# Kernel tuning notes

Hardware: AMD Instinct MI355X
Metric: run time of the kernel (lower is better)

The kernel has to match this reference:

```python
import jax, jax.numpy as jnp
import numpy as np

N = 8192      # number of graph nodes
C = 256       # feature_size
D = C // 2    # projection dim


def setup_inputs() -> dict:
    key = jax.random.key(0)
    ks = jax.random.split(key, 10)
    s_in = 1.0 / np.sqrt(C + 3)   # torch Linear default init scale (uniform bound)
    s_r = 1.0 / np.sqrt(D)
    return {
        "landmarks": jax.random.normal(ks[0], (1, N, 3), dtype=jnp.float32),
        "features": jax.random.normal(ks[1], (1, N, C), dtype=jnp.float32),
        # weights stored [in, out]
        "Wi": jax.random.uniform(ks[2], (C + 3, D), jnp.float32, -s_in, s_in),
        "bi": jax.random.uniform(ks[3], (D,), jnp.float32, -s_in, s_in),
        "Wj": jax.random.uniform(ks[4], (C + 3, D), jnp.float32, -s_in, s_in),
        "bj": jax.random.uniform(ks[5], (D,), jnp.float32, -s_in, s_in),
        "Wk": jax.random.uniform(ks[6], (C + 3, D), jnp.float32, -s_in, s_in),
        "bk": jax.random.uniform(ks[7], (D,), jnp.float32, -s_in, s_in),
        "Wr": jax.random.uniform(ks[8], (D, C), jnp.float32, -s_r, s_r),
        "br": jax.random.uniform(ks[9], (C,), jnp.float32, -s_r, s_r),
    }


def reference(landmarks, features, Wi, bi, Wj, bj, Wk, bk, Wr, br):
    # concat coords + features, drop the singleton batch dim: [N, C+3]
    x = jnp.concatenate([landmarks, features], axis=2)[0]
    fi = x @ Wi + bi                       # [N, D]
    fj = x @ Wj + bj                       # [N, D]
    fk = x @ Wk + bk                       # [N, D]
    att = jax.nn.sigmoid(fi @ fj.T)        # [N, N] sigmoid scores (non-softmax)
    att = att / jnp.sum(att, axis=1, keepdims=True)  # row-sum normalize
    out = (att @ fk) @ Wr + br             # [N, C] restored
    return features + out[None]            # residual, back to [1, N, C]
```

## Files before the change

kernel.cpp:

```cpp
#include <hip/hip_runtime.h>
#include <stdint.h>

#define N_NODES 8192
#define KPAD 272
#define OUTC 384

typedef __attribute__((ext_vector_type(8))) short bhalf8;
typedef __attribute__((ext_vector_type(16))) float f32x16;
typedef __attribute__((ext_vector_type(4))) float f32x4;

__device__ inline unsigned short f2bf_rne(float f) {
    unsigned u = __builtin_bit_cast(unsigned, f);
    u += 0x7FFFu + ((u >> 16) & 1u);
    return (unsigned short)(u >> 16);
}

__device__ inline bhalf8 mk8(unsigned a, unsigned b, unsigned c, unsigned d) {
    union { unsigned u[4]; bhalf8 v; } U;
    U.u[0] = a; U.u[1] = b; U.u[2] = c; U.u[3] = d;
    return U.v;
}

#define GLD_TO_LDS(gptr, lptr)                                                              \
    __builtin_amdgcn_global_load_lds((const __attribute__((address_space(1))) void*)(gptr), \
                                     (__attribute__((address_space(3))) void*)(lptr), 16, 0, 0)

__global__ void k_prep(const float* __restrict__ landmarks, const float* __restrict__ features,
                       const float* __restrict__ Wi, const float* __restrict__ bi,
                       const float* __restrict__ Wj, const float* __restrict__ bj,
                       const float* __restrict__ Wk, const float* __restrict__ bk,
                       const float* __restrict__ Wr,
                       unsigned short* __restrict__ xb, unsigned short* __restrict__ WcatT,
                       unsigned short* __restrict__ WrT, float* __restrict__ bcat) {
    int idx = blockIdx.x * 256 + threadIdx.x;
    const int XB_N = N_NODES * KPAD;
    const int WC_N = OUTC * KPAD;
    const int WR_N = 256 * 128;
    if (idx < XB_N) {
        int i = idx / KPAD, kk = idx - i * KPAD;
        float v = 0.f;
        if (kk < 256) v = features[i * 256 + kk];
        else if (kk < 259) v = landmarks[i * 3 + (kk - 256)];
        xb[idx] = f2bf_rne(v);
        return;
    }
    idx -= XB_N;
    if (idx < WC_N) {
        int n = idx / KPAD, kk = idx - n * KPAD;
        int sel = n >> 7, d = n & 127;
        const float* W = (sel == 0) ? Wi : ((sel == 1) ? Wj : Wk);
        float v = 0.f;
        if (kk < 256) v = W[(kk + 3) * 128 + d];
        else if (kk < 259) v = W[(kk - 256) * 128 + d];
        WcatT[idx] = f2bf_rne(v);
        return;
    }
    idx -= WC_N;
    if (idx < WR_N) {
        int c = idx >> 7, d = idx & 127;
        WrT[idx] = f2bf_rne(Wr[d * 256 + c]);
        return;
    }
    idx -= WR_N;
    if (idx < OUTC) {
        float v = (idx < 128) ? bi[idx] : ((idx < 256) ? bj[idx - 128] : bk[idx - 256]);
        bcat[idx] = v;
    }
}

__global__ __launch_bounds__(256) void k_proj(const unsigned short* __restrict__ xb,
                                              const unsigned short* __restrict__ WcatT,
                                              const float* __restrict__ bcat,
                                              unsigned short* __restrict__ fi,
                                              unsigned short* __restrict__ fj,
                                              unsigned short* __restrict__ fkT) {
    const int tid = threadIdx.x;
    const int w = tid >> 6, l = tid & 63, h = l >> 5, ln = l & 31;
    const int i0 = blockIdx.x * 32;
    f32x16 acc[3] = {};
#pragma unroll
    for (int s = 0; s < 17; ++s) {
        bhalf8 a = *(const bhalf8*)(xb + (size_t)(i0 + ln) * KPAD + s * 16 + h * 8);
#pragma unroll
        for (int t = 0; t < 3; ++t) {
            int n = 96 * w + 32 * t + ln;
            bhalf8 b = *(const bhalf8*)(WcatT + (size_t)n * KPAD + s * 16 + h * 8);
            acc[t] = __builtin_amdgcn_mfma_f32_32x32x16_bf16(a, b, acc[t], 0, 0, 0);
        }
    }
#pragma unroll
    for (int t = 0; t < 3; ++t) {
        int n = 96 * w + 32 * t + ln;
        int sel = n >> 7, d = n & 127;
        float bias = bcat[n];
#pragma unroll
        for (int q = 0; q < 4; ++q) {
            int ib = i0 + 8 * q + 4 * h;
            if (sel < 2) {
                unsigned short* dst = sel ? fj : fi;
#pragma unroll
                for (int r = 0; r < 4; ++r)
                    dst[(size_t)(ib + r) * 128 + d] = f2bf_rne(acc[t][4 * q + r] + bias);
            } else {
                ushort4 pk;
                pk.x = f2bf_rne(acc[t][4 * q + 0] + bias);
                pk.y = f2bf_rne(acc[t][4 * q + 1] + bias);
                pk.z = f2bf_rne(acc[t][4 * q + 2] + bias);
                pk.w = f2bf_rne(acc[t][4 * q + 3] + bias);
                *(ushort4*)(fkT + (size_t)d * N_NODES + ib) = pk;
            }
        }
    }
}

__global__ __launch_bounds__(256, 2) void k_attn(const unsigned short* __restrict__ fi,
                                                 const unsigned short* __restrict__ fj,
                                                 const unsigned short* __restrict__ fkT,
                                                 float* __restrict__ num_part,
                                                 float* __restrict__ den_part) {
    __shared__ __align__(16) char smem[65536];
    unsigned short* fj_s = (unsigned short*)smem;
    unsigned short* fk_s = (unsigned short*)(smem + 32768);
    float* bufA = (float*)smem;
    float* bufB = (float*)(smem + 17408);
    float* denb = (float*)(smem + 34816);

    const int tid = threadIdx.x;
    const int w = tid >> 6, l = tid & 63, h = l >> 5, ln = l & 31;
    const int rt = blockIdx.x & 127, jq = blockIdx.x >> 7;
    const int i0 = rt * 64;
    const int jbase = jq * 2048;

    bhalf8 bfi[2][8];
#pragma unroll
    for (int nt = 0; nt < 2; ++nt)
#pragma unroll
        for (int s = 0; s < 8; ++s)
            bfi[nt][s] = *(const bhalf8*)(fi + (size_t)(i0 + nt * 32 + ln) * 128 + s * 16 + h * 8);

    f32x16 acc[8] = {};
    float dacc0 = 0.f, dacc1 = 0.f;

    const int rsub = l >> 4;
    const int cph = l & 15;

    for (int mt = 0; mt < 16; ++mt) {
        const int j0 = jbase + mt * 128;
#pragma unroll
        for (int q = 0; q < 8; ++q) {
            int r = w * 32 + q * 4 + rsub;
            int c = cph ^ (r & 15);
            GLD_TO_LDS(fj + (size_t)(j0 + r) * 128 + c * 8, (char*)fj_s + (w * 32 + q * 4) * 256);
            GLD_TO_LDS(fkT + (size_t)r * N_NODES + j0 + c * 8, (char*)fk_s + (w * 32 + q * 4) * 256);
        }
        __syncthreads();

        f32x16 st0 = {}, st1 = {};
        const int jrow = w * 32 + ln;
#pragma unroll
        for (int s = 0; s < 8; ++s) {
            int c = (s * 2 + h) ^ (jrow & 15);
            bhalf8 af = *(const bhalf8*)((char*)fj_s + jrow * 256 + c * 16);
            st0 = __builtin_amdgcn_mfma_f32_32x32x16_bf16(af, bfi[0][s], st0, 0, 0, 0);
            st1 = __builtin_amdgcn_mfma_f32_32x32x16_bf16(af, bfi[1][s], st1, 0, 0, 0);
        }

        float sv0[16], sv1[16];
#pragma unroll
        for (int r = 0; r < 16; ++r) {
            float x0 = __builtin_amdgcn_rcpf(1.f + __builtin_amdgcn_exp2f(st0[r] * -1.44269504f));
            float x1 = __builtin_amdgcn_rcpf(1.f + __builtin_amdgcn_exp2f(st1[r] * -1.44269504f));
            dacc0 += x0; dacc1 += x1;
            sv0[r] = x0; sv1[r] = x1;
        }
        unsigned p0[8], p1[8], x0v[8], x1v[8];
#pragma unroll
        for (int q = 0; q < 8; ++q) {
            p0[q] = __builtin_amdgcn_perm(__builtin_bit_cast(unsigned, sv0[2 * q + 1]),
                                          __builtin_bit_cast(unsigned, sv0[2 * q]), 0x07060302u);
            p1[q] = __builtin_amdgcn_perm(__builtin_bit_cast(unsigned, sv1[2 * q + 1]),
                                          __builtin_bit_cast(unsigned, sv1[2 * q]), 0x07060302u);
        }
#pragma unroll
        for (int q = 0; q < 8; ++q) {
            x0v[q] = (unsigned)__shfl_xor((int)p0[q], 32, 64);
            x1v[q] = (unsigned)__shfl_xor((int)p1[q], 32, 64);
        }
        bhalf8 fb[2][2];
        if (h == 0) {
            fb[0][0] = mk8(p0[0], p0[1], x0v[0], x0v[1]);
            fb[0][1] = mk8(p0[4], p0[5], x0v[4], x0v[5]);
            fb[1][0] = mk8(p1[0], p1[1], x1v[0], x1v[1]);
            fb[1][1] = mk8(p1[4], p1[5], x1v[4], x1v[5]);
        } else {
            fb[0][0] = mk8(x0v[2], x0v[3], p0[2], p0[3]);
            fb[0][1] = mk8(x0v[6], x0v[7], p0[6], p0[7]);
            fb[1][0] = mk8(x1v[2], x1v[3], p1[2], p1[3]);
            fb[1][1] = mk8(x1v[6], x1v[7], p1[6], p1[7]);
        }
#pragma unroll
        for (int m4 = 0; m4 < 4; ++m4) {
#pragma unroll
            for (int s2 = 0; s2 < 2; ++s2) {
                int row = m4 * 32 + ln;
                int c = (w * 4 + s2 * 2 + h) ^ (row & 15);
                bhalf8 af = *(const bhalf8*)((char*)fk_s + row * 256 + c * 16);
                acc[m4 * 2 + 0] = __builtin_amdgcn_mfma_f32_32x32x16_bf16(af, fb[0][s2], acc[m4 * 2 + 0], 0, 0, 0);
                acc[m4 * 2 + 1] = __builtin_amdgcn_mfma_f32_32x32x16_bf16(af, fb[1][s2], acc[m4 * 2 + 1], 0, 0, 0);
            }
        }
        __syncthreads();
    }

    {
        float o0 = __shfl_xor(dacc0, 32, 64);
        float o1 = __shfl_xor(dacc1, 32, 64);
        dacc0 += o0; dacc1 += o1;
    }
    if (h == 0) {
        denb[w * 64 + ln] = dacc0;
        denb[w * 64 + 32 + ln] = dacc1;
    }

#pragma unroll
    for (int half = 0; half < 2; ++half) {
        __syncthreads();
        if (w < 2) {
            float* buf = w ? bufB : bufA;
#pragma unroll
            for (int m2 = 0; m2 < 2; ++m2) {
                int m4 = half * 2 + m2;
#pragma unroll
                for (int nt = 0; nt < 2; ++nt) {
                    int iloc = nt * 32 + ln;
#pragma unroll
                    for (int q = 0; q < 4; ++q) {
                        int d = m2 * 32 + 8 * q + 4 * h;
                        f32x4 v = {acc[m4 * 2 + nt][4 * q + 0], acc[m4 * 2 + nt][4 * q + 1],
                                   acc[m4 * 2 + nt][4 * q + 2], acc[m4 * 2 + nt][4 * q + 3]};
                        *(f32x4*)(buf + iloc * 68 + d) = v;
                    }
                }
            }
        }
        __syncthreads();
        if (w >= 2) {
            float* buf = (w == 3) ? bufB : bufA;
#pragma unroll
            for (int m2 = 0; m2 < 2; ++m2) {
                int m4 = half * 2 + m2;
#pragma unroll
                for (int nt = 0; nt < 2; ++nt) {
                    int iloc = nt * 32 + ln;
#pragma unroll
                    for (int q = 0; q < 4; ++q) {
                        int d = m2 * 32 + 8 * q + 4 * h;
                        f32x4 old = *(f32x4*)(buf + iloc * 68 + d);
                        f32x4 v = {acc[m4 * 2 + nt][4 * q + 0], acc[m4 * 2 + nt][4 * q + 1],
                                   acc[m4 * 2 + nt][4 * q + 2], acc[m4 * 2 + nt][4 * q + 3]};
                        *(f32x4*)(buf + iloc * 68 + d) = old + v;
                    }
                }
            }
        }
        __syncthreads();
#pragma unroll
        for (int e = 0; e < 4; ++e) {
            int v = e * 256 + tid;
            int iloc = v >> 4;
            int d4 = (v & 15) * 4;
            f32x4 s = *(f32x4*)(bufA + iloc * 68 + d4) + *(f32x4*)(bufB + iloc * 68 + d4);
            *(f32x4*)(num_part + (size_t)(jq * N_NODES + i0 + iloc) * 128 + half * 64 + d4) = s;
        }
    }
    __syncthreads();
    if (tid < 64) {
        den_part[(size_t)jq * N_NODES + i0 + tid] =
            denb[tid] + denb[64 + tid] + denb[128 + tid] + denb[192 + tid];
    }
}

__global__ void k_comb(const float* __restrict__ num_part, const float* __restrict__ den_part,
                       unsigned short* __restrict__ t) {
    int f = blockIdx.x * 256 + threadIdx.x;
    int i = f >> 5, d4 = (f & 31) * 4;
    f32x4 s = {};
    float ds = 0.f;
#pragma unroll
    for (int q = 0; q < 4; ++q) {
        s += *(const f32x4*)(num_part + (size_t)(q * N_NODES + i) * 128 + d4);
        ds += den_part[(size_t)q * N_NODES + i];
    }
    float inv = 1.0f / ds;
    ushort4 pk;
    pk.x = f2bf_rne(s.x * inv);
    pk.y = f2bf_rne(s.y * inv);
    pk.z = f2bf_rne(s.z * inv);
    pk.w = f2bf_rne(s.w * inv);
    *(ushort4*)(t + (size_t)i * 128 + d4) = pk;
}

__global__ __launch_bounds__(256) void k_out(const unsigned short* __restrict__ t,
                                             const unsigned short* __restrict__ WrT,
                                             const float* __restrict__ br,
                                             const float* __restrict__ features,
                                             float* __restrict__ out) {
    __shared__ __align__(16) char smem[65536];
    const int tid = threadIdx.x, w = tid >> 6, l = tid & 63, h = l >> 5, ln = l & 31;
    const int i0 = blockIdx.x * 32;
    {
        int rsub = l >> 4, cph = l & 15;
#pragma unroll
        for (int q = 0; q < 16; ++q) {
            int r = w * 64 + q * 4 + rsub;
            int c = cph ^ (r & 15);
            GLD_TO_LDS(WrT + (size_t)r * 128 + c * 8, (char*)smem + (w * 64 + q * 4) * 256);
        }
    }
    __syncthreads();
    f32x16 acc[2] = {};
#pragma unroll
    for (int s = 0; s < 8; ++s) {
        bhalf8 af = *(const bhalf8*)(t + (size_t)(i0 + ln) * 128 + s * 16 + h * 8);
#pragma unroll
        for (int nt = 0; nt < 2; ++nt) {
            int row = w * 64 + nt * 32 + ln;
            int c = (s * 2 + h) ^ (row & 15);
            bhalf8 bf = *(const bhalf8*)((char*)smem + row * 256 + c * 16);
            acc[nt] = __builtin_amdgcn_mfma_f32_32x32x16_bf16(af, bf, acc[nt], 0, 0, 0);
        }
    }
#pragma unroll
    for (int nt = 0; nt < 2; ++nt) {
        int cc = w * 64 + nt * 32 + ln;
        float bias = br[cc];
#pragma unroll
        for (int q = 0; q < 4; ++q) {
#pragma unroll
            for (int r = 0; r < 4; ++r) {
                int i = i0 + 8 * q + 4 * h + r;
                out[(size_t)i * 256 + cc] = acc[nt][4 * q + r] + bias + features[(size_t)i * 256 + cc];
            }
        }
    }
}

extern "C" void kernel_launch(void* const* d_in, const int* in_sizes, int n_in,
                              void* d_out, int out_size, void* d_ws, size_t ws_size,
                              hipStream_t stream) {
    const float* landmarks = (const float*)d_in[0];
    const float* features  = (const float*)d_in[1];
    const float* Wi = (const float*)d_in[2];
    const float* bi = (const float*)d_in[3];
    const float* Wj = (const float*)d_in[4];
    const float* bj = (const float*)d_in[5];
    const float* Wk = (const float*)d_in[6];
    const float* bk = (const float*)d_in[7];
    const float* Wr = (const float*)d_in[8];
    const float* br = (const float*)d_in[9];

    char* ws = (char*)d_ws;
    unsigned short* xb      = (unsigned short*)(ws + 0);
    unsigned short* WcatT   = (unsigned short*)(ws + 4456448);
    unsigned short* WrT     = (unsigned short*)(ws + 4665344);
    float*          bcat    = (float*)(ws + 4730880);
    unsigned short* fi      = (unsigned short*)(ws + 4732416);
    unsigned short* fjp     = (unsigned short*)(ws + 6829568);
    unsigned short* fkT     = (unsigned short*)(ws + 8926720);
    float*          num_part= (float*)(ws + 11023872);
    float*          den_part= (float*)(ws + 27801088);
    unsigned short* t       = (unsigned short*)(ws + 27932160);

    float* out = (float*)d_out;

    hipLaunchKernelGGL(k_prep, dim3(9242), dim3(256), 0, stream,
                       landmarks, features, Wi, bi, Wj, bj, Wk, bk, Wr, xb, WcatT, WrT, bcat);
    hipLaunchKernelGGL(k_proj, dim3(256), dim3(256), 0, stream, xb, WcatT, bcat, fi, fjp, fkT);
    hipLaunchKernelGGL(k_attn, dim3(512), dim3(256), 0, stream, fi, fjp, fkT, num_part, den_part);
    hipLaunchKernelGGL(k_comb, dim3(1024), dim3(256), 0, stream, num_part, den_part, t);
    hipLaunchKernelGGL(k_out, dim3(256), dim3(256), 0, stream, t, WrT, br, features, out);
}
```

Measured before the change: 183.5 us.

## Fuse input cast into projection, double-buffer attention, fold combine into output GEMM

```diff
diff --git a/kernel.cpp b/kernel.cpp
--- a/kernel.cpp
+++ b/kernel.cpp
@@ -25,26 +25,15 @@
     __builtin_amdgcn_global_load_lds((const __attribute__((address_space(1))) void*)(gptr), \
                                      (__attribute__((address_space(3))) void*)(lptr), 16, 0, 0)
 
-__global__ void k_prep(const float* __restrict__ landmarks, const float* __restrict__ features,
-                       const float* __restrict__ Wi, const float* __restrict__ bi,
+__global__ void k_prep(const float* __restrict__ Wi, const float* __restrict__ bi,
                        const float* __restrict__ Wj, const float* __restrict__ bj,
                        const float* __restrict__ Wk, const float* __restrict__ bk,
                        const float* __restrict__ Wr,
-                       unsigned short* __restrict__ xb, unsigned short* __restrict__ WcatT,
-                       unsigned short* __restrict__ WrT, float* __restrict__ bcat) {
+                       unsigned short* __restrict__ WcatT, unsigned short* __restrict__ WrT,
+                       float* __restrict__ bcat) {
     int idx = blockIdx.x * 256 + threadIdx.x;
-    const int XB_N = N_NODES * KPAD;
     const int WC_N = OUTC * KPAD;
     const int WR_N = 256 * 128;
-    if (idx < XB_N) {
-        int i = idx / KPAD, kk = idx - i * KPAD;
-        float v = 0.f;
-        if (kk < 256) v = features[i * 256 + kk];
-        else if (kk < 259) v = landmarks[i * 3 + (kk - 256)];
-        xb[idx] = f2bf_rne(v);
-        return;
-    }
-    idx -= XB_N;
     if (idx < WC_N) {
         int n = idx / KPAD, kk = idx - n * KPAD;
         int sel = n >> 7, d = n & 127;
@@ -68,47 +57,62 @@
     }
 }
 
-__global__ __launch_bounds__(256) void k_proj(const unsigned short* __restrict__ xb,
+__global__ __launch_bounds__(256) void k_proj(const float* __restrict__ landmarks,
+                                              const float* __restrict__ features,
                                               const unsigned short* __restrict__ WcatT,
                                               const float* __restrict__ bcat,
                                               unsigned short* __restrict__ fi,
                                               unsigned short* __restrict__ fj,
                                               unsigned short* __restrict__ fkT) {
-    const int tid = threadIdx.x;
-    const int w = tid >> 6, l = tid & 63, h = l >> 5, ln = l & 31;
-    const int i0 = blockIdx.x * 32;
-    f32x16 acc[3] = {};
+    const int tid = threadIdx.x, w = tid >> 6, l = tid & 63, h = l >> 5, ln = l & 31;
+    const unsigned bid = blockIdx.x;
+    const int it = bid / 3, ng = bid - it * 3;
+    const int i0 = it * 32;
+    const int n = ng * 128 + w * 32 + ln;
+    const int row = i0 + ln;
+    f32x16 acc = {};
 #pragma unroll
     for (int s = 0; s < 17; ++s) {
-        bhalf8 a = *(const bhalf8*)(xb + (size_t)(i0 + ln) * KPAD + s * 16 + h * 8);
-#pragma unroll
-        for (int t = 0; t < 3; ++t) {
-            int n = 96 * w + 32 * t + ln;
-            bhalf8 b = *(const bhalf8*)(WcatT + (size_t)n * KPAD + s * 16 + h * 8);
-            acc[t] = __builtin_amdgcn_mfma_f32_32x32x16_bf16(a, b, acc[t], 0, 0, 0);
-        }
-    }
-#pragma unroll
-    for (int t = 0; t < 3; ++t) {
-        int n = 96 * w + 32 * t + ln;
-        int sel = n >> 7, d = n & 127;
-        float bias = bcat[n];
+        union { unsigned short us[8]; bhalf8 v; } A;
+        if (s < 16) {
+            const float* fp = features + (size_t)row * 256 + s * 16 + h * 8;
+            f32x4 v0 = *(const f32x4*)(fp);
+            f32x4 v1 = *(const f32x4*)(fp + 4);
+#pragma unroll
+            for (int e = 0; e < 4; ++e) { A.us[e] = f2bf_rne(v0[e]); A.us[4 + e] = f2bf_rne(v1[e]); }
+        } else {
+#pragma unroll
+            for (int e = 0; e < 8; ++e) A.us[e] = 0;
+            if (h == 0) {
+                A.us[0] = f2bf_rne(landmarks[row * 3 + 0]);
+                A.us[1] = f2bf_rne(landmarks[row * 3 + 1]);
+                A.us[2] = f2bf_rne(landmarks[row * 3 + 2]);
+            }
+        }
+        bhalf8 b = *(const bhalf8*)(WcatT + (size_t)n * KPAD + s * 16 + h * 8);
+        acc = __builtin_amdgcn_mfma_f32_32x32x16_bf16(A.v, b, acc, 0, 0, 0);
+    }
+    const int d = w * 32 + ln;
+    const float bias = bcat[n];
+    if (ng < 2) {
+        unsigned short* dst = ng ? fj : fi;
 #pragma unroll
         for (int q = 0; q < 4; ++q) {
             int ib = i0 + 8 * q + 4 * h;
-            if (sel < 2) {
-                unsigned short* dst = sel ? fj : fi;
-#pragma unroll
-                for (int r = 0; r < 4; ++r)
-                    dst[(size_t)(ib + r) * 128 + d] = f2bf_rne(acc[t][4 * q + r] + bias);
-            } else {
-                ushort4 pk;
-                pk.x = f2bf_rne(acc[t][4 * q + 0] + bias);
-                pk.y = f2bf_rne(acc[t][4 * q + 1] + bias);
-                pk.z = f2bf_rne(acc[t][4 * q + 2] + bias);
-                pk.w = f2bf_rne(acc[t][4 * q + 3] + bias);
-                *(ushort4*)(fkT + (size_t)d * N_NODES + ib) = pk;
-            }
+#pragma unroll
+            for (int r = 0; r < 4; ++r)
+                dst[(size_t)(ib + r) * 128 + d] = f2bf_rne(acc[4 * q + r] + bias);
+        }
+    } else {
+#pragma unroll
+        for (int q = 0; q < 4; ++q) {
+            int ib = i0 + 8 * q + 4 * h;
+            ushort4 pk;
+            pk.x = f2bf_rne(acc[4 * q + 0] + bias);
+            pk.y = f2bf_rne(acc[4 * q + 1] + bias);
+            pk.z = f2bf_rne(acc[4 * q + 2] + bias);
+            pk.w = f2bf_rne(acc[4 * q + 3] + bias);
+            *(ushort4*)(fkT + (size_t)d * N_NODES + ib) = pk;
         }
     }
 }
@@ -119,52 +123,59 @@
                                                  float* __restrict__ num_part,
                                                  float* __restrict__ den_part) {
     __shared__ __align__(16) char smem[65536];
-    unsigned short* fj_s = (unsigned short*)smem;
-    unsigned short* fk_s = (unsigned short*)(smem + 32768);
-    float* bufA = (float*)smem;
-    float* bufB = (float*)(smem + 17408);
-    float* denb = (float*)(smem + 34816);
+    char* const fjb0 = smem;
+    char* const fkb0 = smem + 16384;
+    char* const fjb1 = smem + 32768;
+    char* const fkb1 = smem + 49152;
 
     const int tid = threadIdx.x;
     const int w = tid >> 6, l = tid & 63, h = l >> 5, ln = l & 31;
-    const int rt = blockIdx.x & 127, jq = blockIdx.x >> 7;
-    const int i0 = rt * 64;
-    const int jbase = jq * 2048;
+    const int ih = w >> 1, jh = w & 1;
+    const int rt = blockIdx.x & 63, jq = blockIdx.x >> 6;
+    const int i0 = rt * 128;
+    const int jbase = jq * 1024;
+
+    const int rsub = l >> 4, cph = l & 15;
 
     bhalf8 bfi[2][8];
 #pragma unroll
     for (int nt = 0; nt < 2; ++nt)
 #pragma unroll
         for (int s = 0; s < 8; ++s)
-            bfi[nt][s] = *(const bhalf8*)(fi + (size_t)(i0 + nt * 32 + ln) * 128 + s * 16 + h * 8);
+            bfi[nt][s] = *(const bhalf8*)(fi + (size_t)(i0 + ih * 64 + nt * 32 + ln) * 128 + s * 16 + h * 8);
 
     f32x16 acc[8] = {};
     float dacc0 = 0.f, dacc1 = 0.f;
 
-    const int rsub = l >> 4;
-    const int cph = l & 15;
-
-    for (int mt = 0; mt < 16; ++mt) {
-        const int j0 = jbase + mt * 128;
-#pragma unroll
-        for (int q = 0; q < 8; ++q) {
-            int r = w * 32 + q * 4 + rsub;
+    auto STAGE = [&](char* fjd, char* fkd, int J0) {
+#pragma unroll
+        for (int q = 0; q < 4; ++q) {
+            int r = w * 16 + q * 4 + rsub;
             int c = cph ^ (r & 15);
-            GLD_TO_LDS(fj + (size_t)(j0 + r) * 128 + c * 8, (char*)fj_s + (w * 32 + q * 4) * 256);
-            GLD_TO_LDS(fkT + (size_t)r * N_NODES + j0 + c * 8, (char*)fk_s + (w * 32 + q * 4) * 256);
-        }
-        __syncthreads();
-
+            GLD_TO_LDS(fj + (size_t)(J0 + r) * 128 + c * 8, fjd + (w * 16 + q * 4) * 256);
+        }
+#pragma unroll
+        for (int q = 0; q < 4; ++q) {
+            int r = w * 16 + q * 4 + rsub;
+            int g = cph ^ (r & 15);
+            int d = r + ((g >> 3) << 6);
+            int joff = (g & 7) * 8;
+            GLD_TO_LDS(fkT + (size_t)d * N_NODES + J0 + joff, fkd + (w * 16 + q * 4) * 256);
+        }
+    };
+
+    auto COMPUTE = [&](const char* fjbuf, const char* fkbuf) {
         f32x16 st0 = {}, st1 = {};
-        const int jrow = w * 32 + ln;
+        const int jrow = jh * 32 + ln;
+        __builtin_amdgcn_s_setprio(1);
 #pragma unroll
         for (int s = 0; s < 8; ++s) {
             int c = (s * 2 + h) ^ (jrow & 15);
-            bhalf8 af = *(const bhalf8*)((char*)fj_s + jrow * 256 + c * 16);
+            bhalf8 af = *(const bhalf8*)(fjbuf + jrow * 256 + c * 16);
             st0 = __builtin_amdgcn_mfma_f32_32x32x16_bf16(af, bfi[0][s], st0, 0, 0, 0);
             st1 = __builtin_amdgcn_mfma_f32_32x32x16_bf16(af, bfi[1][s], st1, 0, 0, 0);
         }
-
+        __builtin_amdgcn_s_setprio(0);
         float sv0[16], sv1[16];
 #pragma unroll
         for (int r = 0; r < 16; ++r) {
@@ -198,114 +209,108 @@
             fb[1][0] = mk8(x1v[2], x1v[3], p1[2], p1[3]);
             fb[1][1] = mk8(x1v[6], x1v[7], p1[6], p1[7]);
         }
+        __builtin_amdgcn_s_setprio(1);
 #pragma unroll
         for (int m4 = 0; m4 < 4; ++m4) {
+            int d = m4 * 32 + ln;
+            int r = d & 63;
+            int ghi = (d >> 6) << 3;
 #pragma unroll
             for (int s2 = 0; s2 < 2; ++s2) {
-                int row = m4 * 32 + ln;
-                int c = (w * 4 + s2 * 2 + h) ^ (row & 15);
-                bhalf8 af = *(const bhalf8*)((char*)fk_s + row * 256 + c * 16);
+                int g = ghi | (jh * 4 + s2 * 2 + h);
+                int slot = g ^ (r & 15);
+                bhalf8 af = *(const bhalf8*)(fkbuf + r * 256 + slot * 16);
                 acc[m4 * 2 + 0] = __builtin_amdgcn_mfma_f32_32x32x16_bf16(af, fb[0][s2], acc[m4 * 2 + 0], 0, 0, 0);
                 acc[m4 * 2 + 1] = __builtin_amdgcn_mfma_f32_32x32x16_bf16(af, fb[1][s2], acc[m4 * 2 + 1], 0, 0, 0);
             }
         }
+        __builtin_amdgcn_s_setprio(0);
+    };
+
+    STAGE(fjb0, fkb0, jbase);
+    __syncthreads();
+#pragma unroll 1
+    for (int mt = 0; mt < 16; mt += 2) {
+        STAGE(fjb1, fkb1, jbase + (mt + 1) * 64);
+        COMPUTE(fjb0, fkb0);
         __syncthreads();
-    }
-
-    {
-        float o0 = __shfl_xor(dacc0, 32, 64);
-        float o1 = __shfl_xor(dacc1, 32, 64);
-        dacc0 += o0; dacc1 += o1;
-    }
+        if (mt + 2 < 16) STAGE(fjb0, fkb0, jbase + (mt + 2) * 64);
+        COMPUTE(fjb1, fkb1);
+        __syncthreads();
+    }
+
+    dacc0 += __shfl_xor(dacc0, 32, 64);
+    dacc1 += __shfl_xor(dacc1, 32, 64);
+    float* denb = (float*)(smem + 34816);
     if (h == 0) {
-        denb[w * 64 + ln] = dacc0;
-        denb[w * 64 + 32 + ln] = dacc1;
-    }
-
+        denb[jh * 128 + ih * 64 + ln] = dacc0;
+        denb[jh * 128 + ih * 64 + 32 + ln] = dacc1;
+    }
+
+    float* buf = (float*)smem;
 #pragma unroll
     for (int half = 0; half < 2; ++half) {
         __syncthreads();
-        if (w < 2) {
-            float* buf = w ? bufB : bufA;
+        if (jh == 0) {
 #pragma unroll
             for (int m2 = 0; m2 < 2; ++m2) {
                 int m4 = half * 2 + m2;
 #pragma unroll
                 for (int nt = 0; nt < 2; ++nt) {
-                    int iloc = nt * 32 + ln;
+                    int irow = ih * 64 + nt * 32 + ln;
 #pragma unroll
                     for (int q = 0; q < 4; ++q) {
-                        int d = m2 * 32 + 8 * q + 4 * h;
+                        int dd = m2 * 32 + 8 * q + 4 * h;
                         f32x4 v = {acc[m4 * 2 + nt][4 * q + 0], acc[m4 * 2 + nt][4 * q + 1],
                                    acc[m4 * 2 + nt][4 * q + 2], acc[m4 * 2 + nt][4 * q + 3]};
-                        *(f32x4*)(buf + iloc * 68 + d) = v;
+                        *(f32x4*)(buf + irow * 68 + dd) = v;
                     }
                 }
             }
         }
         __syncthreads();
-        if (w >= 2) {
-            float* buf = (w == 3) ? bufB : bufA;
+        if (jh == 1) {
 #pragma unroll
             for (int m2 = 0; m2 < 2; ++m2) {
                 int m4 = half * 2 + m2;
 #pragma unroll
                 for (int nt = 0; nt < 2; ++nt) {
-                    int iloc = nt * 32 + ln;
+                    int irow = ih * 64 + nt * 32 + ln;
 #pragma unroll
                     for (int q = 0; q < 4; ++q) {
-                        int d = m2 * 32 + 8 * q + 4 * h;
-                        f32x4 old = *(f32x4*)(buf + iloc * 68 + d);
+                        int dd = m2 * 32 + 8 * q + 4 * h;
+                        float* p4 = buf + irow * 68 + dd;
+                        f32x4 old = *(f32x4*)p4;
                         f32x4 v = {acc[m4 * 2 + nt][4 * q + 0], acc[m4 * 2 + nt][4 * q + 1],
                                    acc[m4 * 2 + nt][4 * q + 2], acc[m4 * 2 + nt][4 * q + 3]};
-                        *(f32x4*)(buf + iloc * 68 + d) = old + v;
+                        *(f32x4*)p4 = old + v;
                     }
                 }
             }
         }
         __syncthreads();
 #pragma unroll
-        for (int e = 0; e < 4; ++e) {
+        for (int e = 0; e < 8; ++e) {
             int v = e * 256 + tid;
-            int iloc = v >> 4;
-            int d4 = (v & 15) * 4;
-            f32x4 s = *(f32x4*)(bufA + iloc * 68 + d4) + *(f32x4*)(bufB + iloc * 68 + d4);
-            *(f32x4*)(num_part + (size_t)(jq * N_NODES + i0 + iloc) * 128 + half * 64 + d4) = s;
+            int iloc = v >> 4, dq = v & 15;
+            *(f32x4*)(num_part + ((size_t)(jq * N_NODES + i0 + iloc)) * 128 + half * 64 + dq * 4) =
+                *(const f32x4*)(buf + iloc * 68 + dq * 4);
         }
     }
     __syncthreads();
-    if (tid < 64) {
-        den_part[(size_t)jq * N_NODES + i0 + tid] =
-            denb[tid] + denb[64 + tid] + denb[128 + tid] + denb[192 + tid];
-    }
-}
-
-__global__ void k_comb(const float* __restrict__ num_part, const float* __restrict__ den_part,
-                       unsigned short* __restrict__ t) {
-    int f = blockIdx.x * 256 + threadIdx.x;
-    int i = f >> 5, d4 = (f & 31) * 4;
-    f32x4 s = {};
-    float ds = 0.f;
-#pragma unroll
-    for (int q = 0; q < 4; ++q) {
-        s += *(const f32x4*)(num_part + (size_t)(q * N_NODES + i) * 128 + d4);
-        ds += den_part[(size_t)q * N_NODES + i];
-    }
-    float inv = 1.0f / ds;
-    ushort4 pk;
-    pk.x = f2bf_rne(s.x * inv);
-    pk.y = f2bf_rne(s.y * inv);
-    pk.z = f2bf_rne(s.z * inv);
-    pk.w = f2bf_rne(s.w * inv);
-    *(ushort4*)(t + (size_t)i * 128 + d4) = pk;
-}
-
-__global__ __launch_bounds__(256) void k_out(const unsigned short* __restrict__ t,
-                                             const unsigned short* __restrict__ WrT,
+    if (tid < 128) {
+        den_part[(size_t)jq * N_NODES + i0 + tid] = denb[tid] + denb[128 + tid];
+    }
+}
+
+__global__ __launch_bounds__(256) void k_out(const unsigned short* __restrict__ WrT,
                                              const float* __restrict__ br,
                                              const float* __restrict__ features,
+                                             const float* __restrict__ num_part,
+                                             const float* __restrict__ den_part,
                                              float* __restrict__ out) {
-    __shared__ __align__(16) char smem[65536];
+    __shared__ __align__(16) char smem[73728];
+    char* const tb = smem + 65536;
     const int tid = threadIdx.x, w = tid >> 6, l = tid & 63, h = l >> 5, ln = l & 31;
     const int i0 = blockIdx.x * 32;
     {
@@ -314,19 +319,46 @@
         for (int q = 0; q < 16; ++q) {
             int r = w * 64 + q * 4 + rsub;
             int c = cph ^ (r & 15);
-            GLD_TO_LDS(WrT + (size_t)r * 128 + c * 8, (char*)smem + (w * 64 + q * 4) * 256);
+            GLD_TO_LDS(WrT + (size_t)r * 128 + c * 8, smem + (w * 64 + q * 4) * 256);
+        }
+    }
+    {
+        int i = tid >> 3, dseg = (tid & 7) * 16;
+        f32x4 s[4] = {};
+        float ds = 0.f;
+#pragma unroll
+        for (int q = 0; q < 8; ++q) {
+            const float* np = num_part + ((size_t)(q * N_NODES + i0 + i)) * 128 + dseg;
+#pragma unroll
+            for (int k = 0; k < 4; ++k) s[k] += *(const f32x4*)(np + 4 * k);
+            ds += den_part[(size_t)q * N_NODES + i0 + i];
+        }
+        float inv = 1.0f / ds;
+#pragma unroll
+        for (int cc = 0; cc < 2; ++cc) {
+            union { unsigned u[4]; bhalf8 v; } U;
+#pragma unroll
+            for (int m = 0; m < 4; ++m) {
+                int e0 = cc * 8 + 2 * m;
+                unsigned lo = f2bf_rne(s[e0 >> 2][e0 & 3] * inv);
+                unsigned hi = f2bf_rne(s[(e0 + 1) >> 2][(e0 + 1) & 3] * inv);
+                U.u[m] = lo | (hi << 16);
+            }
+            int slot = ((tid & 7) * 2 + cc) ^ (i & 15);
+            *(bhalf8*)(tb + i * 256 + slot * 16) = U.v;
         }
     }
     __syncthreads();
     f32x16 acc[2] = {};
 #pragma unroll
     for (int s = 0; s < 8; ++s) {
-        bhalf8 af = *(const bhalf8*)(t + (size_t)(i0 + ln) * 128 + s * 16 + h * 8);
+        int ca = (s * 2 + h) ^ (ln & 15);
+        bhalf8 af = *(const bhalf8*)(tb + ln * 256 + ca * 16);
 #pragma unroll
         for (int nt = 0; nt < 2; ++nt) {
             int row = w * 64 + nt * 32 + ln;
             int c = (s * 2 + h) ^ (row & 15);
-            bhalf8 bf = *(const bhalf8*)((char*)smem + row * 256 + c * 16);
+            bhalf8 bf = *(const bhalf8*)(smem + row * 256 + c * 16);
             acc[nt] = __builtin_amdgcn_mfma_f32_32x32x16_bf16(af, bf, acc[nt], 0, 0, 0);
         }
     }
@@ -360,23 +392,22 @@
     const float* br = (const float*)d_in[9];
 
     char* ws = (char*)d_ws;
-    unsigned short* xb      = (unsigned short*)(ws + 0);
-    unsigned short* WcatT   = (unsigned short*)(ws + 4456448);
-    unsigned short* WrT     = (unsigned short*)(ws + 4665344);
-    float*          bcat    = (float*)(ws + 4730880);
-    unsigned short* fi      = (unsigned short*)(ws + 4732416);
-    unsigned short* fjp     = (unsigned short*)(ws + 6829568);
-    unsigned short* fkT     = (unsigned short*)(ws + 8926720);
-    float*          num_part= (float*)(ws + 11023872);
-    float*          den_part= (float*)(ws + 27801088);
-    unsigned short* t       = (unsigned short*)(ws + 27932160);
+    unsigned short* WcatT   = (unsigned short*)(ws + 0);
+    unsigned short* WrT     = (unsigned short*)(ws + 208896);
+    float*          bcat    = (float*)(ws + 274432);
+    unsigned short* fi      = (unsigned short*)(ws + 275968);
+    unsigned short* fjp     = (unsigned short*)(ws + 2373120);
+    unsigned short* fkT     = (unsigned short*)(ws + 4470272);
+    float*          num_part= (float*)(ws + 6567424);
+    float*          den_part= (float*)(ws + 40121856);
 
     float* out = (float*)d_out;
 
-    hipLaunchKernelGGL(k_prep, dim3(9242), dim3(256), 0, stream,
-                       landmarks, features, Wi, bi, Wj, bj, Wk, bk, Wr, xb, WcatT, WrT, bcat);
-    hipLaunchKernelGGL(k_proj, dim3(256), dim3(256), 0, stream, xb, WcatT, bcat, fi, fjp, fkT);
+    hipLaunchKernelGGL(k_prep, dim3(538), dim3(256), 0, stream,
+                       Wi, bi, Wj, bj, Wk, bk, Wr, WcatT, WrT, bcat);
+    hipLaunchKernelGGL(k_proj, dim3(768), dim3(256), 0, stream,
+                       landmarks, features, WcatT, bcat, fi, fjp, fkT);
     hipLaunchKernelGGL(k_attn, dim3(512), dim3(256), 0, stream, fi, fjp, fkT, num_part, den_part);
-    hipLaunchKernelGGL(k_comb, dim3(1024), dim3(256), 0, stream, num_part, den_part, t);
-    hipLaunchKernelGGL(k_out, dim3(256), dim3(256), 0, stream, t, WrT, br, features, out);
-}
+    hipLaunchKernelGGL(k_out, dim3(256), dim3(256), 0, stream,
+                       WrT, br, features, num_part, den_part, out);
+}
```

Result: slower. 198.7 us (+8.3%).
